# Kernel tuning notes

Measured on AMD Instinct MI355X. Metric: run time of the kernel, lower is better.

Reference implementation:

```python
import jax, jax.numpy as jnp
import numpy as np

B, N, M, D, H = 2, 256, 64, 768, 12
HD = D // H  # head dim 64


def setup_inputs() -> dict:
    key = jax.random.key(0)
    ks = jax.random.split(key, 8)
    s = 0.02
    return {
        "x": jax.random.normal(ks[0], (B, N, D), jnp.float32),
        "sim_embeddings": jax.random.normal(ks[1], (B, N, M, D), jnp.float32),
        "Wq": jax.random.normal(ks[2], (D, D), jnp.float32) * s,
        "bq": jnp.zeros((D,), jnp.float32),
        "Wkv": jax.random.normal(ks[3], (D, 2 * D), jnp.float32) * s,
        "bkv": jnp.zeros((2 * D,), jnp.float32),
        "Wp": jax.random.normal(ks[4], (D, D), jnp.float32) * s,
        "bp": jnp.zeros((D,), jnp.float32),
    }


def reference(x, sim_embeddings, Wq, bq, Wkv, bkv, Wp, bp):
    # x: (B,N,D); sim_embeddings: (B,N,M,D)
    b, n, d = x.shape
    m = sim_embeddings.shape[2]
    scale = HD ** -0.5

    q = (x @ Wq + bq).reshape(b, n, H, HD).transpose(0, 2, 1, 3)  # (B,H,N,hd)

    kv_x = x @ Wkv + bkv                       # (B,N,2D)
    k_x, v_x = jnp.split(kv_x, 2, axis=-1)
    k_x = k_x.reshape(b, n, H, HD).transpose(0, 2, 1, 3)  # (B,H,N,hd) shared-global K
    v_x = v_x.reshape(b, n, H, HD).transpose(0, 2, 1, 3)

    kv_s = sim_embeddings @ Wkv + bkv          # (B,N,M,2D)
    k_s, v_s = jnp.split(kv_s, 2, axis=-1)
    k_s = k_s.reshape(b, n, m, H, HD).transpose(0, 3, 1, 2, 4)  # (B,H,N,M,hd) per-query local K
    v_s = v_s.reshape(b, n, m, H, HD).transpose(0, 3, 1, 2, 4)

    # scores over concatenated [global N keys | local M keys] without expanding K to (B,N,N+M,D)
    sg = jnp.einsum('bhnd,bhkd->bhnk', q, k_x) * scale   # (B,H,N,N)
    sl = jnp.einsum('bhnd,bhnmd->bhnm', q, k_s) * scale  # (B,H,N,M)
    attn = jax.nn.softmax(jnp.concatenate([sg, sl], axis=-1), axis=-1)
    ag, al = attn[..., :n], attn[..., n:]

    out = (jnp.einsum('bhnk,bhkd->bhnd', ag, v_x)
           + jnp.einsum('bhnm,bhnmd->bhnd', al, v_s))   # (B,H,N,hd)
    out = out.transpose(0, 2, 1, 3).reshape(b, n, d)
    return out @ Wp + bp
```

## Files before the change

kernel.cpp:

```cpp
#include <hip/hip_runtime.h>
#include <stdint.h>

#define DEV_INLINE __device__ __forceinline__

typedef __bf16 bf16x8 __attribute__((ext_vector_type(8)));
typedef float f32x4 __attribute__((ext_vector_type(4)));

typedef const __attribute__((address_space(1))) void* gas_ptr;
typedef __attribute__((address_space(3))) void* las_ptr;

DEV_INLINE unsigned short f2bf(float f) {
    union { float f; unsigned u; } v; v.f = f;
    unsigned r = v.u + 0x7fffu + ((v.u >> 16) & 1u);
    return (unsigned short)(r >> 16);
}
DEV_INLINE float bf2f(unsigned short u) {
    union { unsigned u; float f; } v; v.u = ((unsigned)u) << 16;
    return v.f;
}


__global__ void cast_bf16_kernel(const float* __restrict__ src,
                                 unsigned short* __restrict__ dst, long n4) {
    long i = (long)blockIdx.x * blockDim.x + threadIdx.x;
    if (i >= n4) return;
    float4 a = ((const float4*)src)[i];
    ushort4 o;
    o.x = f2bf(a.x); o.y = f2bf(a.y); o.z = f2bf(a.z); o.w = f2bf(a.w);
    ((ushort4*)dst)[i] = o;
}

__global__ void transpose_cast_kernel(const float* __restrict__ src, int C,
                                      unsigned short* __restrict__ dst, int ld_dst) {
    __shared__ float t[64][65];
    int c0 = blockIdx.x * 64, r0 = blockIdx.y * 64;
    int tx = threadIdx.x, ty = threadIdx.y;
    #pragma unroll
    for (int i = 0; i < 64; i += 16)
        t[ty + i][tx] = src[(long)(r0 + ty + i) * C + c0 + tx];
    __syncthreads();
    #pragma unroll
    for (int i = 0; i < 64; i += 16)
        dst[(long)(c0 + ty + i) * ld_dst + r0 + tx] = f2bf(t[tx][ty + i]);
}

__global__ void bias_init_kernel(const float* __restrict__ bq,
                                 const float* __restrict__ bkv,
                                 float* __restrict__ bias1,
                                 float* __restrict__ zerobuf) {
    int i = blockIdx.x * 256 + threadIdx.x;
    if (i < 2304) bias1[i] = (i < 768) ? bq[i] : bkv[i - 768];
    else if (i < 3072) zerobuf[i - 2304] = 0.f;
}


template <int WM, int WN, int WAVES_M, int OUT, bool CIN, bool G1E>
__global__ __launch_bounds__(256)
void gemm_bf16_kernel(const unsigned short* __restrict__ A, int lda,
                      const unsigned short* __restrict__ BT, int ldb,
                      const float* __restrict__ bias,
                      void* __restrict__ Cout, int ldc, int K,
                      const float* __restrict__ cin,
                      long aZb, long aZh, long bZb, long bZh, long oZb, long oZh,
                      float* __restrict__ g1_qf, unsigned short* __restrict__ g1_qb,
                      unsigned short* __restrict__ g1_kxb,
                      unsigned short* __restrict__ g1_vxT) {
    constexpr int TR = WAVES_M * WM * 16;
    constexpr int TC = (4 / WAVES_M) * WN * 16;
    __shared__ unsigned short As[TR * 64];
    __shared__ unsigned short Bs[TC * 64];
    const int tid = threadIdx.x;
    const int w = tid >> 6, lane = tid & 63;
    const int lm = lane & 15, quad = lane >> 4;
    const int z = blockIdx.z;
    const int zb = z / 12, zh = z % 12;
    A  += zb * aZb + zh * aZh;
    BT += zb * bZb + zh * bZh;
    const long obase = zb * oZb + zh * oZh;
    const long tm = (long)blockIdx.y * TR;
    const long tn = (long)blockIdx.x * TC;
    const int m_off = (w % WAVES_M) * WM * 16;
    const int n_off = (w / WAVES_M) * WN * 16;
    const int lrow8 = lane >> 3;
    const int lcol_sw = (((lane & 7) ^ lrow8) * 8);

    f32x4 acc[WM][WN];
    #pragma unroll
    for (int mi = 0; mi < WM; ++mi)
        #pragma unroll
        for (int ni = 0; ni < WN; ++ni) acc[mi][ni] = f32x4{0.f, 0.f, 0.f, 0.f};

    for (int k0 = 0; k0 < K; k0 += 64) {
        __syncthreads();
        #pragma unroll
        for (int i = 0; i < TR / 32; ++i) {
            int r0 = w * (TR / 4) + i * 8;
            const unsigned short* ga = A + (tm + r0 + lrow8) * lda + k0 + lcol_sw;
            __builtin_amdgcn_global_load_lds((gas_ptr)ga, (las_ptr)(As + r0 * 64), 16, 0, 0);
        }
        #pragma unroll
        for (int i = 0; i < TC / 32; ++i) {
            int r0 = w * (TC / 4) + i * 8;
            const unsigned short* gb = BT + (tn + r0 + lrow8) * ldb + k0 + lcol_sw;
            __builtin_amdgcn_global_load_lds((gas_ptr)gb, (las_ptr)(Bs + r0 * 64), 16, 0, 0);
        }
        __syncthreads();
        #pragma unroll
        for (int kk = 0; kk < 2; ++kk) {
            bf16x8 af[WM], bfr[WN];
            #pragma unroll
            for (int mi = 0; mi < WM; ++mi) {
                int r = m_off + mi * 16 + lm;
                af[mi] = *(const bf16x8*)(As + r * 64 + (((kk * 4 + quad) ^ (r & 7)) * 8));
            }
            #pragma unroll
            for (int ni = 0; ni < WN; ++ni) {
                int r = n_off + ni * 16 + lm;
                bfr[ni] = *(const bf16x8*)(Bs + r * 64 + (((kk * 4 + quad) ^ (r & 7)) * 8));
            }
            #pragma unroll
            for (int mi = 0; mi < WM; ++mi)
                #pragma unroll
                for (int ni = 0; ni < WN; ++ni)
                    acc[mi][ni] = __builtin_amdgcn_mfma_f32_16x16x32_bf16(
                        af[mi], bfr[ni], acc[mi][ni], 0, 0, 0);
        }
    }

    #pragma unroll
    for (int mi = 0; mi < WM; ++mi) {
        #pragma unroll
        for (int ni = 0; ni < WN; ++ni) {
            long col = tn + n_off + ni * 16 + lm;
            float bv = bias[col];
            #pragma unroll
            for (int r = 0; r < 4; ++r) {
                long row = tm + m_off + mi * 16 + quad * 4 + r;
                float v = acc[mi][ni][r] + bv;
                if (G1E) {
                    if (col < 768) {
                        g1_qf[row * 768 + col] = v;
                        g1_qb[row * 768 + col] = f2bf(v);
                    } else if (col < 1536) {
                        g1_kxb[row * 768 + (col - 768)] = f2bf(v);
                    } else {
                        int j = (int)col - 1536, h = j >> 6, d = j & 63;
                        int bb = (int)row >> 8, n = (int)row & 255;
                        g1_vxT[((long)(bb * 12 + h) * 64 + d) * 256 + n] = f2bf(v);
                    }
                } else {
                    long idx = obase + row * ldc + col;
                    if (CIN) v += cin[idx];
                    if (OUT == 0) ((float*)Cout)[idx] = v;
                    else ((unsigned short*)Cout)[idx] = f2bf(v);
                }
            }
        }
    }
}

__global__ __launch_bounds__(256)
void attn_fused_kernel(const float* __restrict__ sim,
                       const unsigned short* __restrict__ qWb,
                       const float* __restrict__ qf,
                       const float* __restrict__ bkv,
                       const float* __restrict__ sgbuf,
                       unsigned short* __restrict__ agb,
                       float* __restrict__ outg0,
                       unsigned short* __restrict__ simbar) {
    __shared__ unsigned short qw_s[16 * 784];
    __shared__ unsigned short sim_s[64 * 64];
    __shared__ float q_l[768];
    __shared__ float slb_s[12];
    __shared__ float scl[12][68];
    __shared__ float al_s[12][64];

    const int t = threadIdx.x;
    const int lane = t & 63, w = t >> 6;
    const int lm = lane & 15, quad = lane >> 4;
    const int n = blockIdx.x, b = blockIdx.y;
    const int n_ = b * 256 + n;
    const float* simn = sim + (long)n_ * 49152;

    {
        const int h = t >> 4, c0 = t & 15;
        const unsigned short* src = qWb + ((long)h * 512 + n_) * 768;
        #pragma unroll
        for (int j = 0; j < 6; ++j) {
            int ch = c0 + 16 * j;
            *(bf16x8*)(qw_s + h * 784 + ch * 8) = *(const bf16x8*)(src + ch * 8);
        }
    }
    q_l[t] = qf[(long)n_ * 768 + t];
    q_l[t + 256] = qf[(long)n_ * 768 + t + 256];
    q_l[t + 512] = qf[(long)n_ * 768 + t + 512];
    __syncthreads();
    if (t < 12) {
        float s = 0.f;
        #pragma unroll 8
        for (int d = 0; d < 64; ++d) s += q_l[t * 64 + d] * bkv[t * 64 + d];
        slb_s[t] = s;
    }

    f32x4 acc = {};
    for (int k0 = 0; k0 < 768; k0 += 64) {
        __syncthreads();
        #pragma unroll
        for (int i = 0; i < 2; ++i) {
            int id = t + 256 * i;
            int r = id >> 3, q = id & 7;
            const float* gp = simn + r * 768 + k0 + q * 8;
            float4 a = *(const float4*)gp;
            float4 c = *(const float4*)(gp + 4);
            union { bf16x8 v; unsigned short u[8]; } pk;
            pk.u[0] = f2bf(a.x); pk.u[1] = f2bf(a.y);
            pk.u[2] = f2bf(a.z); pk.u[3] = f2bf(a.w);
            pk.u[4] = f2bf(c.x); pk.u[5] = f2bf(c.y);
            pk.u[6] = f2bf(c.z); pk.u[7] = f2bf(c.w);
            *(bf16x8*)(sim_s + r * 64 + ((q ^ (r & 7)) * 8)) = pk.v;
        }
        __syncthreads();
        #pragma unroll
        for (int kk = 0; kk < 2; ++kk) {
            int r = w * 16 + lm;
            bf16x8 af = *(const bf16x8*)(sim_s + r * 64 + (((kk * 4 + quad) ^ (r & 7)) * 8));
            bf16x8 bf_ = *(const bf16x8*)(qw_s + lm * 784 + k0 + kk * 32 + quad * 8);
            acc = __builtin_amdgcn_mfma_f32_16x16x32_bf16(af, bf_, acc, 0, 0, 0);
        }
    }
    if (lm < 12) {
        #pragma unroll
        for (int r = 0; r < 4; ++r)
            scl[lm][w * 16 + quad * 4 + r] = (acc[r] + slb_s[lm]) * 0.125f;
    }
    __syncthreads();

    #pragma unroll
    for (int i = 0; i < 3; ++i) {
        const int h = w * 3 + i;
        const float* sgr = sgbuf + (long)(b * 12 + h) * 65536 + (long)n * 256;
        float v0 = sgr[lane] * 0.125f, v1 = sgr[lane + 64] * 0.125f,
              v2 = sgr[lane + 128] * 0.125f, v3 = sgr[lane + 192] * 0.125f;
        float v4 = scl[h][lane];
        float mx = fmaxf(fmaxf(fmaxf(v0, v1), fmaxf(v2, v3)), v4);
        #pragma unroll
        for (int off = 32; off > 0; off >>= 1) mx = fmaxf(mx, __shfl_xor(mx, off));
        float e0 = __expf(v0 - mx), e1 = __expf(v1 - mx), e2 = __expf(v2 - mx),
              e3 = __expf(v3 - mx), e4 = __expf(v4 - mx);
        float s = e0 + e1 + e2 + e3 + e4;
        #pragma unroll
        for (int off = 32; off > 0; off >>= 1) s += __shfl_xor(s, off);
        float inv = __frcp_rn(s);
        unsigned short* agr = agb + (long)(b * 12 + h) * 65536 + (long)n * 256;
        agr[lane] = f2bf(e0 * inv); agr[lane + 64] = f2bf(e1 * inv);
        agr[lane + 128] = f2bf(e2 * inv); agr[lane + 192] = f2bf(e3 * inv);
        float al = e4 * inv;
        al_s[h][lane] = al;
        float am = al;
        #pragma unroll
        for (int off = 32; off > 0; off >>= 1) am += __shfl_xor(am, off);
        outg0[(long)n_ * 768 + h * 64 + lane] = am * bkv[768 + h * 64 + lane];
    }
    __syncthreads();

    float a0[12], a1[12], a2[12];
    #pragma unroll
    for (int h = 0; h < 12; ++h) { a0[h] = 0.f; a1[h] = 0.f; a2[h] = 0.f; }
    for (int m = 0; m < 64; ++m) {
        float s0 = simn[(long)m * 768 + t];
        float s1 = simn[(long)m * 768 + t + 256];
        float s2 = simn[(long)m * 768 + t + 512];
        #pragma unroll
        for (int h = 0; h < 12; ++h) {
            float a = al_s[h][m];
            a0[h] += a * s0; a1[h] += a * s1; a2[h] += a * s2;
        }
    }
    #pragma unroll
    for (int h = 0; h < 12; ++h) {
        unsigned short* dst = simbar + ((long)h * 512 + n_) * 768;
        dst[t] = f2bf(a0[h]);
        dst[t + 256] = f2bf(a1[h]);
        dst[t + 512] = f2bf(a2[h]);
    }
}


extern "C" void kernel_launch(void* const* d_in, const int* in_sizes, int n_in,
                              void* d_out, int out_size, void* d_ws, size_t ws_size,
                              hipStream_t stream) {
    const float* x   = (const float*)d_in[0];
    const float* sim = (const float*)d_in[1];
    const float* Wq  = (const float*)d_in[2];
    const float* bq  = (const float*)d_in[3];
    const float* Wkv = (const float*)d_in[4];
    const float* bkv = (const float*)d_in[5];
    const float* Wp  = (const float*)d_in[6];
    const float* bp  = (const float*)d_in[7];
    float* out = (float*)d_out;

    char* ws = (char*)d_ws;
    size_t off = 0;
    auto alloc = [&](size_t bytes) {
        char* p = ws + off;
        off += (bytes + 255) & ~(size_t)255;
        return p;
    };
    unsigned short* xb     = (unsigned short*)alloc(512UL * 768 * 2);
    unsigned short* w1t    = (unsigned short*)alloc(2304UL * 768 * 2);
    unsigned short* wkvb   = (unsigned short*)alloc(768UL * 1536 * 2);
    unsigned short* wpt    = (unsigned short*)alloc(768UL * 768 * 2);
    float*          qf     = (float*)alloc(512UL * 768 * 4);
    unsigned short* qb     = (unsigned short*)alloc(512UL * 768 * 2);
    unsigned short* kxb    = (unsigned short*)alloc(512UL * 768 * 2);
    unsigned short* vxT    = (unsigned short*)alloc(24UL * 64 * 256 * 2);
    unsigned short* qWb    = (unsigned short*)alloc(16UL * 512 * 768 * 2);
    float*          sgbuf  = (float*)alloc(24UL * 65536 * 4);
    unsigned short* agb    = (unsigned short*)alloc(24UL * 65536 * 2);
    float*          outg0  = (float*)alloc(512UL * 768 * 4);
    float*          outg   = (float*)alloc(512UL * 768 * 4);
    unsigned short* simbar = (unsigned short*)alloc(12UL * 512 * 768 * 2);
    unsigned short* attnb  = (unsigned short*)alloc(512UL * 768 * 2);
    float*          bias1  = (float*)alloc(2304UL * 4);
    float*          zbuf   = (float*)alloc(768UL * 4);

    cast_bf16_kernel<<<384, 256, 0, stream>>>(x, xb, 512L * 768 / 4);
    cast_bf16_kernel<<<1152, 256, 0, stream>>>(Wkv, wkvb, 768L * 1536 / 4);
    transpose_cast_kernel<<<dim3(12, 12), dim3(64, 16), 0, stream>>>(Wq, 768, w1t, 768);
    transpose_cast_kernel<<<dim3(24, 12), dim3(64, 16), 0, stream>>>(Wkv, 1536, w1t + 768L * 768, 768);
    transpose_cast_kernel<<<dim3(12, 12), dim3(64, 16), 0, stream>>>(Wp, 768, wpt, 768);
    bias_init_kernel<<<12, 256, 0, stream>>>(bq, bkv, bias1, zbuf);

    gemm_bf16_kernel<2, 2, 2, 0, false, true><<<dim3(36, 8, 1), 256, 0, stream>>>(
        xb, 768, w1t, 768, bias1, nullptr, 768, 768, nullptr,
        0, 0, 0, 0, 0, 0, qf, qb, kxb, vxT);

    gemm_bf16_kernel<2, 2, 2, 1, false, false><<<dim3(12, 8, 12), 256, 0, stream>>>(
        qb, 768, wkvb, 1536, zbuf, qWb, 768, 64, nullptr,
        0, 64, 0, 64, 0, 512L * 768, nullptr, nullptr, nullptr, nullptr);

    gemm_bf16_kernel<2, 2, 2, 0, false, false><<<dim3(4, 4, 24), 256, 0, stream>>>(
        qb, 768, kxb, 768, zbuf, sgbuf, 256, 64, nullptr,
        196608, 64, 196608, 64, 786432, 65536, nullptr, nullptr, nullptr, nullptr);

    attn_fused_kernel<<<dim3(256, 2), 256, 0, stream>>>(
        sim, qWb, qf, bkv, sgbuf, agb, outg0, simbar);

    gemm_bf16_kernel<2, 2, 2, 0, true, false><<<dim3(1, 4, 24), 256, 0, stream>>>(
        agb, 256, vxT, 256, zbuf, outg, 768, 256, outg0,
        786432, 65536, 196608, 16384, 196608, 64, nullptr, nullptr, nullptr, nullptr);

    gemm_bf16_kernel<2, 2, 2, 1, true, false><<<dim3(1, 8, 12), 256, 0, stream>>>(
        simbar, 768, w1t + 1536L * 768, 768, zbuf, attnb, 768, 768, outg,
        0, 393216, 0, 49152, 0, 64, nullptr, nullptr, nullptr, nullptr);

    gemm_bf16_kernel<2, 2, 2, 0, false, false><<<dim3(12, 8, 1), 256, 0, stream>>>(
        attnb, 768, wpt, 768, bp, out, 768, 768, nullptr,
        0, 0, 0, 0, 0, 0, nullptr, nullptr, nullptr, nullptr);
}
```

Before: 252.5 us.

## Merge prep kernels, fuse GEMMs, split simbar, register-prefetch sim tiles

Collapses the cast, transpose and bias kernels into two launches. It merges the qW and sg GEMMs into one grid and fuses the ag·V and simbar·Wv GEMMs into a single concatenated-K GEMM, with smaller tiles for more blocks. The simbar weighted sum moves out of the attention kernel into its own kernel that spreads columns across more blocks. The attention kernel now double-buffers sim tiles through register prefetch with one barrier per chunk. The aim is fewer launches, more parallelism and hidden global-load latency, at the cost of an extra al_g round-trip through global memory and a second full read of sim.

```diff
diff --git a/kernel.cpp b/kernel.cpp
--- a/kernel.cpp
+++ b/kernel.cpp
@@ -14,71 +14,73 @@
     unsigned r = v.u + 0x7fffu + ((v.u >> 16) & 1u);
     return (unsigned short)(r >> 16);
 }
-DEV_INLINE float bf2f(unsigned short u) {
-    union { unsigned u; float f; } v; v.u = ((unsigned)u) << 16;
-    return v.f;
-}
-
-
-__global__ void cast_bf16_kernel(const float* __restrict__ src,
-                                 unsigned short* __restrict__ dst, long n4) {
-    long i = (long)blockIdx.x * blockDim.x + threadIdx.x;
-    if (i >= n4) return;
-    float4 a = ((const float4*)src)[i];
-    ushort4 o;
-    o.x = f2bf(a.x); o.y = f2bf(a.y); o.z = f2bf(a.z); o.w = f2bf(a.w);
-    ((ushort4*)dst)[i] = o;
-}
-
-__global__ void transpose_cast_kernel(const float* __restrict__ src, int C,
-                                      unsigned short* __restrict__ dst, int ld_dst) {
-    __shared__ float t[64][65];
-    int c0 = blockIdx.x * 64, r0 = blockIdx.y * 64;
+
+DEV_INLINE void lds_barrier() {
+    __builtin_amdgcn_sched_barrier(0);
+    asm volatile("s_waitcnt lgkmcnt(0)" ::: "memory");
+    __builtin_amdgcn_s_barrier();
+    __builtin_amdgcn_sched_barrier(0);
+}
+
+__global__ __launch_bounds__(256)
+void prep_cast_kernel(const float* __restrict__ x, unsigned short* __restrict__ xb,
+                      const float* __restrict__ Wkv, unsigned short* __restrict__ wkvb,
+                      const float* __restrict__ bq, const float* __restrict__ bkv,
+                      float* __restrict__ bias1, float* __restrict__ zbuf) {
+    int bid = blockIdx.x;
+    if (bid < 1536) {
+        const float* s; unsigned short* d; long i;
+        if (bid < 384) { s = x;   d = xb;   i = (long)bid * 256 + threadIdx.x; }
+        else           { s = Wkv; d = wkvb; i = (long)(bid - 384) * 256 + threadIdx.x; }
+        float4 a = ((const float4*)s)[i];
+        ushort4 o;
+        o.x = f2bf(a.x); o.y = f2bf(a.y); o.z = f2bf(a.z); o.w = f2bf(a.w);
+        ((ushort4*)d)[i] = o;
+    } else {
+        int i = (bid - 1536) * 256 + threadIdx.x;
+        if (i < 768) bias1[i] = bq[i];
+        else if (i < 2304) bias1[i] = bkv[i - 768];
+        else zbuf[i - 2304] = 0.f;
+    }
+}
+
+__global__ void transpose3_kernel(const float* __restrict__ Wq,
+                                  const float* __restrict__ Wkv,
+                                  const float* __restrict__ Wp,
+                                  unsigned short* __restrict__ w1t,
+                                  unsigned short* __restrict__ wpt) {
+    __shared__ float tl[64][65];
+    int bx = blockIdx.x;
+    const float* src; unsigned short* dst; int C;
+    if (bx < 12)      { src = Wq;  dst = w1t;              C = 768; }
+    else if (bx < 36) { src = Wkv; dst = w1t + 768L * 768; C = 1536; bx -= 12; }
+    else              { src = Wp;  dst = wpt;              C = 768; bx -= 36; }
+    int c0 = bx * 64, r0 = blockIdx.y * 64;
     int tx = threadIdx.x, ty = threadIdx.y;
     #pragma unroll
     for (int i = 0; i < 64; i += 16)
-        t[ty + i][tx] = src[(long)(r0 + ty + i) * C + c0 + tx];
+        tl[ty + i][tx] = src[(long)(r0 + ty + i) * C + c0 + tx];
     __syncthreads();
     #pragma unroll
     for (int i = 0; i < 64; i += 16)
-        dst[(long)(c0 + ty + i) * ld_dst + r0 + tx] = f2bf(t[tx][ty + i]);
-}
-
-__global__ void bias_init_kernel(const float* __restrict__ bq,
-                                 const float* __restrict__ bkv,
-                                 float* __restrict__ bias1,
-                                 float* __restrict__ zerobuf) {
-    int i = blockIdx.x * 256 + threadIdx.x;
-    if (i < 2304) bias1[i] = (i < 768) ? bq[i] : bkv[i - 768];
-    else if (i < 3072) zerobuf[i - 2304] = 0.f;
-}
-
-
-template <int WM, int WN, int WAVES_M, int OUT, bool CIN, bool G1E>
-__global__ __launch_bounds__(256)
-void gemm_bf16_kernel(const unsigned short* __restrict__ A, int lda,
-                      const unsigned short* __restrict__ BT, int ldb,
-                      const float* __restrict__ bias,
-                      void* __restrict__ Cout, int ldc, int K,
-                      const float* __restrict__ cin,
-                      long aZb, long aZh, long bZb, long bZh, long oZb, long oZh,
-                      float* __restrict__ g1_qf, unsigned short* __restrict__ g1_qb,
-                      unsigned short* __restrict__ g1_kxb,
-                      unsigned short* __restrict__ g1_vxT) {
+        dst[(long)(c0 + ty + i) * 768 + r0 + tx] = f2bf(tl[tx][ty + i]);
+}
+
+template <int WM, int WN, int WAVES_M, bool G1E>
+DEV_INLINE void gemm_body(const unsigned short* A, int lda,
+                          const unsigned short* BT, int ldb,
+                          const unsigned short* A2, int lda2,
+                          const unsigned short* B2, int ldb2, int K1,
+                          const float* bias, void* Cout, int ldc, int K,
+                          const float* cin, int OUT, long obase, long tm, long tn,
+                          unsigned short* As, unsigned short* Bs,
+                          float* g1_qf, unsigned short* g1_qb,
+                          unsigned short* g1_kxb, unsigned short* g1_vxT) {
     constexpr int TR = WAVES_M * WM * 16;
     constexpr int TC = (4 / WAVES_M) * WN * 16;
-    __shared__ unsigned short As[TR * 64];
-    __shared__ unsigned short Bs[TC * 64];
     const int tid = threadIdx.x;
     const int w = tid >> 6, lane = tid & 63;
     const int lm = lane & 15, quad = lane >> 4;
-    const int z = blockIdx.z;
-    const int zb = z / 12, zh = z % 12;
-    A  += zb * aZb + zh * aZh;
-    BT += zb * bZb + zh * bZh;
-    const long obase = zb * oZb + zh * oZh;
-    const long tm = (long)blockIdx.y * TR;
-    const long tn = (long)blockIdx.x * TC;
     const int m_off = (w % WAVES_M) * WM * 16;
     const int n_off = (w / WAVES_M) * WN * 16;
     const int lrow8 = lane >> 3;
@@ -91,18 +93,22 @@
         for (int ni = 0; ni < WN; ++ni) acc[mi][ni] = f32x4{0.f, 0.f, 0.f, 0.f};
 
     for (int k0 = 0; k0 < K; k0 += 64) {
+        const unsigned short* Ab; const unsigned short* Bb;
+        int la, lb, kc;
+        if (k0 < K1) { Ab = A;  Bb = BT; la = lda;  lb = ldb;  kc = k0; }
+        else         { Ab = A2; Bb = B2; la = lda2; lb = ldb2; kc = k0 - K1; }
         __syncthreads();
         #pragma unroll
         for (int i = 0; i < TR / 32; ++i) {
-            int r0 = w * (TR / 4) + i * 8;
-            const unsigned short* ga = A + (tm + r0 + lrow8) * lda + k0 + lcol_sw;
-            __builtin_amdgcn_global_load_lds((gas_ptr)ga, (las_ptr)(As + r0 * 64), 16, 0, 0);
+            int rr = w * (TR / 4) + i * 8;
+            const unsigned short* ga = Ab + (tm + rr + lrow8) * la + kc + lcol_sw;
+            __builtin_amdgcn_global_load_lds((gas_ptr)ga, (las_ptr)(As + rr * 64), 16, 0, 0);
         }
         #pragma unroll
         for (int i = 0; i < TC / 32; ++i) {
-            int r0 = w * (TC / 4) + i * 8;
-            const unsigned short* gb = BT + (tn + r0 + lrow8) * ldb + k0 + lcol_sw;
-            __builtin_amdgcn_global_load_lds((gas_ptr)gb, (las_ptr)(Bs + r0 * 64), 16, 0, 0);
+            int rr = w * (TC / 4) + i * 8;
+            const unsigned short* gb = Bb + (tn + rr + lrow8) * lb + kc + lcol_sw;
+            __builtin_amdgcn_global_load_lds((gas_ptr)gb, (las_ptr)(Bs + rr * 64), 16, 0, 0);
         }
         __syncthreads();
         #pragma unroll
@@ -145,18 +151,96 @@
                         g1_kxb[row * 768 + (col - 768)] = f2bf(v);
                     } else {
                         int j = (int)col - 1536, h = j >> 6, d = j & 63;
-                        int bb = (int)row >> 8, n = (int)row & 255;
-                        g1_vxT[((long)(bb * 12 + h) * 64 + d) * 256 + n] = f2bf(v);
+                        int bb = (int)row >> 8, nn = (int)row & 255;
+                        g1_vxT[((long)(bb * 12 + h) * 64 + d) * 256 + nn] = f2bf(v);
                     }
                 } else {
                     long idx = obase + row * ldc + col;
-                    if (CIN) v += cin[idx];
+                    if (cin) v += cin[idx];
                     if (OUT == 0) ((float*)Cout)[idx] = v;
                     else ((unsigned short*)Cout)[idx] = f2bf(v);
                 }
             }
         }
     }
+}
+
+template <int WM, int WN, int WAVES_M, bool G1E>
+__global__ __launch_bounds__(256)
+void gemm_bf16_kernel(const unsigned short* __restrict__ A, int lda,
+                      const unsigned short* __restrict__ BT, int ldb,
+                      const float* __restrict__ bias,
+                      void* __restrict__ Cout, int ldc, int K,
+                      const float* __restrict__ cin, int OUT,
+                      long aZb, long aZh, long bZb, long bZh, long oZb, long oZh,
+                      float* __restrict__ g1_qf, unsigned short* __restrict__ g1_qb,
+                      unsigned short* __restrict__ g1_kxb,
+                      unsigned short* __restrict__ g1_vxT) {
+    constexpr int TR = WAVES_M * WM * 16;
+    constexpr int TC = (4 / WAVES_M) * WN * 16;
+    __shared__ unsigned short As[TR * 64];
+    __shared__ unsigned short Bs[TC * 64];
+    const int z = blockIdx.z, zb = z / 12, zh = z % 12;
+    gemm_body<WM, WN, WAVES_M, G1E>(
+        A + zb * aZb + zh * aZh, lda, BT + zb * bZb + zh * bZh, ldb,
+        nullptr, 0, nullptr, 0, 1 << 30,
+        bias, Cout, ldc, K, cin, OUT, zb * oZb + zh * oZh,
+        (long)blockIdx.y * TR, (long)blockIdx.x * TC, As, Bs,
+        g1_qf, g1_qb, g1_kxb, g1_vxT);
+}
+
+__global__ __launch_bounds__(256)
+void gemm_qwsg_kernel(const unsigned short* __restrict__ qb,
+                      const unsigned short* __restrict__ wkvb,
+                      const unsigned short* __restrict__ kxb,
+                      const float* __restrict__ zbuf,
+                      unsigned short* __restrict__ qWb,
+                      float* __restrict__ sgbuf) {
+    __shared__ unsigned short As[64 * 64];
+    __shared__ unsigned short Bs[64 * 64];
+    int bid = blockIdx.x;
+    if (bid < 1152) {
+        int bx = bid % 12, by = (bid / 12) % 8, h = bid / 96;
+        gemm_body<2, 2, 2, false>(
+            qb + h * 64, 768, wkvb + h * 64, 1536,
+            nullptr, 0, nullptr, 0, 1 << 30,
+            zbuf, qWb, 768, 64, nullptr, 1, (long)h * 393216,
+            (long)by * 64, (long)bx * 64, As, Bs,
+            nullptr, nullptr, nullptr, nullptr);
+    } else {
+        int bid2 = bid - 1152;
+        int bx = bid2 % 4, by = (bid2 / 4) % 4, z = bid2 / 16;
+        int zb = z / 12, zh = z % 12;
+        gemm_body<2, 2, 2, false>(
+            qb + zb * 196608 + zh * 64, 768, kxb + zb * 196608 + zh * 64, 768,
+            nullptr, 0, nullptr, 0, 1 << 30,
+            zbuf, sgbuf, 256, 64, nullptr, 0,
+            (long)zb * 786432 + (long)zh * 65536,
+            (long)by * 64, (long)bx * 64, As, Bs,
+            nullptr, nullptr, nullptr, nullptr);
+    }
+}
+
+template <int WM, int WN, int WAVES_M>
+__global__ __launch_bounds__(256)
+void gemm_concat_kernel(const unsigned short* __restrict__ A, int lda, long aZb, long aZh,
+                        const unsigned short* __restrict__ BT, int ldb, long bZb, long bZh,
+                        const unsigned short* __restrict__ A2, int lda2, long a2Zb, long a2Zh,
+                        const unsigned short* __restrict__ B2, int ldb2, long b2Zb, long b2Zh,
+                        int K1, int K, const float* __restrict__ bias,
+                        void* __restrict__ Cout, int ldc,
+                        const float* __restrict__ cin, int OUT, long oZb, long oZh) {
+    constexpr int TR = WAVES_M * WM * 16;
+    constexpr int TC = (4 / WAVES_M) * WN * 16;
+    __shared__ unsigned short As[TR * 64];
+    __shared__ unsigned short Bs[TC * 64];
+    const int z = blockIdx.z, zb = z / 12, zh = z % 12;
+    gemm_body<WM, WN, WAVES_M, false>(
+        A + zb * aZb + zh * aZh, lda, BT + zb * bZb + zh * bZh, ldb,
+        A2 + zb * a2Zb + zh * a2Zh, lda2, B2 + zb * b2Zb + zh * b2Zh, ldb2, K1,
+        bias, Cout, ldc, K, cin, OUT, zb * oZb + zh * oZh,
+        (long)blockIdx.y * TR, (long)blockIdx.x * TC, As, Bs,
+        nullptr, nullptr, nullptr, nullptr);
 }
 
 __global__ __launch_bounds__(256)
@@ -167,13 +251,12 @@
                        const float* __restrict__ sgbuf,
                        unsigned short* __restrict__ agb,
                        float* __restrict__ outg0,
-                       unsigned short* __restrict__ simbar) {
+                       float* __restrict__ al_g) {
     __shared__ unsigned short qw_s[16 * 784];
-    __shared__ unsigned short sim_s[64 * 64];
+    __shared__ unsigned short sim_s[2][64 * 64];
     __shared__ float q_l[768];
     __shared__ float slb_s[12];
     __shared__ float scl[12][68];
-    __shared__ float al_s[12][64];
 
     const int t = threadIdx.x;
     const int lane = t & 63, w = t >> 6;
@@ -194,6 +277,15 @@
     q_l[t] = qf[(long)n_ * 768 + t];
     q_l[t + 256] = qf[(long)n_ * 768 + t + 256];
     q_l[t + 512] = qf[(long)n_ * 768 + t + 512];
+
+    const int r0 = t >> 3, q8 = t & 7, r1 = r0 + 32;
+    float4 p0a, p0b, p1a, p1b;
+    {
+        const float* g0 = simn + r0 * 768 + q8 * 8;
+        p0a = *(const float4*)g0; p0b = *(const float4*)(g0 + 4);
+        const float* g1 = simn + r1 * 768 + q8 * 8;
+        p1a = *(const float4*)g1; p1b = *(const float4*)(g1 + 4);
+    }
     __syncthreads();
     if (t < 12) {
         float s = 0.f;
@@ -203,29 +295,34 @@
     }
 
     f32x4 acc = {};
-    for (int k0 = 0; k0 < 768; k0 += 64) {
-        __syncthreads();
-        #pragma unroll
-        for (int i = 0; i < 2; ++i) {
-            int id = t + 256 * i;
-            int r = id >> 3, q = id & 7;
-            const float* gp = simn + r * 768 + k0 + q * 8;
-            float4 a = *(const float4*)gp;
-            float4 c = *(const float4*)(gp + 4);
-            union { bf16x8 v; unsigned short u[8]; } pk;
-            pk.u[0] = f2bf(a.x); pk.u[1] = f2bf(a.y);
-            pk.u[2] = f2bf(a.z); pk.u[3] = f2bf(a.w);
-            pk.u[4] = f2bf(c.x); pk.u[5] = f2bf(c.y);
-            pk.u[6] = f2bf(c.z); pk.u[7] = f2bf(c.w);
-            *(bf16x8*)(sim_s + r * 64 + ((q ^ (r & 7)) * 8)) = pk.v;
-        }
-        __syncthreads();
+    #pragma unroll
+    for (int c = 0; c < 12; ++c) {
+        const int k0 = c * 64;
+        unsigned short* buf = sim_s[c & 1];
+        union { bf16x8 v; unsigned short u[8]; } pk;
+        pk.u[0] = f2bf(p0a.x); pk.u[1] = f2bf(p0a.y);
+        pk.u[2] = f2bf(p0a.z); pk.u[3] = f2bf(p0a.w);
+        pk.u[4] = f2bf(p0b.x); pk.u[5] = f2bf(p0b.y);
+        pk.u[6] = f2bf(p0b.z); pk.u[7] = f2bf(p0b.w);
+        *(bf16x8*)(buf + r0 * 64 + ((q8 ^ (r0 & 7)) * 8)) = pk.v;
+        pk.u[0] = f2bf(p1a.x); pk.u[1] = f2bf(p1a.y);
+        pk.u[2] = f2bf(p1a.z); pk.u[3] = f2bf(p1a.w);
+        pk.u[4] = f2bf(p1b.x); pk.u[5] = f2bf(p1b.y);
+        pk.u[6] = f2bf(p1b.z); pk.u[7] = f2bf(p1b.w);
+        *(bf16x8*)(buf + r1 * 64 + ((q8 ^ (r1 & 7)) * 8)) = pk.v;
+        if (c < 11) {
+            const float* g0 = simn + r0 * 768 + k0 + 64 + q8 * 8;
+            p0a = *(const float4*)g0; p0b = *(const float4*)(g0 + 4);
+            const float* g1 = simn + r1 * 768 + k0 + 64 + q8 * 8;
+            p1a = *(const float4*)g1; p1b = *(const float4*)(g1 + 4);
+        }
+        lds_barrier();
         #pragma unroll
         for (int kk = 0; kk < 2; ++kk) {
             int r = w * 16 + lm;
-            bf16x8 af = *(const bf16x8*)(sim_s + r * 64 + (((kk * 4 + quad) ^ (r & 7)) * 8));
-            bf16x8 bf_ = *(const bf16x8*)(qw_s + lm * 784 + k0 + kk * 32 + quad * 8);
-            acc = __builtin_amdgcn_mfma_f32_16x16x32_bf16(af, bf_, acc, 0, 0, 0);
+            bf16x8 af = *(const bf16x8*)(buf + r * 64 + (((kk * 4 + quad) ^ (r & 7)) * 8));
+            bf16x8 bfr = *(const bf16x8*)(qw_s + lm * 784 + k0 + kk * 32 + quad * 8);
+            acc = __builtin_amdgcn_mfma_f32_16x16x32_bf16(af, bfr, acc, 0, 0, 0);
         }
     }
     if (lm < 12) {
@@ -255,34 +352,39 @@
         agr[lane] = f2bf(e0 * inv); agr[lane + 64] = f2bf(e1 * inv);
         agr[lane + 128] = f2bf(e2 * inv); agr[lane + 192] = f2bf(e3 * inv);
         float al = e4 * inv;
-        al_s[h][lane] = al;
+        al_g[(long)n_ * 768 + h * 64 + lane] = al;
         float am = al;
         #pragma unroll
         for (int off = 32; off > 0; off >>= 1) am += __shfl_xor(am, off);
         outg0[(long)n_ * 768 + h * 64 + lane] = am * bkv[768 + h * 64 + lane];
     }
+}
+
+__global__ __launch_bounds__(256)
+void simbar_kernel(const float* __restrict__ sim,
+                   const float* __restrict__ al_g,
+                   unsigned short* __restrict__ simbar) {
+    __shared__ float al_l[768];
+    const int t = threadIdx.x;
+    const int n_ = blockIdx.x;
+    const int c = blockIdx.y * 256 + t;
+    const float* simn = sim + (long)n_ * 49152;
+    al_l[t] = al_g[(long)n_ * 768 + t];
+    al_l[t + 256] = al_g[(long)n_ * 768 + t + 256];
+    al_l[t + 512] = al_g[(long)n_ * 768 + t + 512];
     __syncthreads();
-
-    float a0[12], a1[12], a2[12];
-    #pragma unroll
-    for (int h = 0; h < 12; ++h) { a0[h] = 0.f; a1[h] = 0.f; a2[h] = 0.f; }
+    float a[12];
+    #pragma unroll
+    for (int h = 0; h < 12; ++h) a[h] = 0.f;
+    #pragma unroll 4
     for (int m = 0; m < 64; ++m) {
-        float s0 = simn[(long)m * 768 + t];
-        float s1 = simn[(long)m * 768 + t + 256];
-        float s2 = simn[(long)m * 768 + t + 512];
-        #pragma unroll
-        for (int h = 0; h < 12; ++h) {
-            float a = al_s[h][m];
-            a0[h] += a * s0; a1[h] += a * s1; a2[h] += a * s2;
-        }
-    }
-    #pragma unroll
-    for (int h = 0; h < 12; ++h) {
-        unsigned short* dst = simbar + ((long)h * 512 + n_) * 768;
-        dst[t] = f2bf(a0[h]);
-        dst[t + 256] = f2bf(a1[h]);
-        dst[t + 512] = f2bf(a2[h]);
-    }
+        float s = simn[(long)m * 768 + c];
+        #pragma unroll
+        for (int h = 0; h < 12; ++h) a[h] += al_l[h * 64 + m] * s;
+    }
+    #pragma unroll
+    for (int h = 0; h < 12; ++h)
+        simbar[((long)h * 512 + n_) * 768 + c] = f2bf(a[h]);
 }
 
 
@@ -318,43 +420,34 @@
     float*          sgbuf  = (float*)alloc(24UL * 65536 * 4);
     unsigned short* agb    = (unsigned short*)alloc(24UL * 65536 * 2);
     float*          outg0  = (float*)alloc(512UL * 768 * 4);
-    float*          outg   = (float*)alloc(512UL * 768 * 4);
+    float*          al_g   = (float*)alloc(512UL * 768 * 4);
     unsigned short* simbar = (unsigned short*)alloc(12UL * 512 * 768 * 2);
     unsigned short* attnb  = (unsigned short*)alloc(512UL * 768 * 2);
     float*          bias1  = (float*)alloc(2304UL * 4);
     float*          zbuf   = (float*)alloc(768UL * 4);
 
-    cast_bf16_kernel<<<384, 256, 0, stream>>>(x, xb, 512L * 768 / 4);
-    cast_bf16_kernel<<<1152, 256, 0, stream>>>(Wkv, wkvb, 768L * 1536 / 4);
-    transpose_cast_kernel<<<dim3(12, 12), dim3(64, 16), 0, stream>>>(Wq, 768, w1t, 768);
-    transpose_cast_kernel<<<dim3(24, 12), dim3(64, 16), 0, stream>>>(Wkv, 1536, w1t + 768L * 768, 768);
-    transpose_cast_kernel<<<dim3(12, 12), dim3(64, 16), 0, stream>>>(Wp, 768, wpt, 768);
-    bias_init_kernel<<<12, 256, 0, stream>>>(bq, bkv, bias1, zbuf);
-
-    gemm_bf16_kernel<2, 2, 2, 0, false, true><<<dim3(36, 8, 1), 256, 0, stream>>>(
-        xb, 768, w1t, 768, bias1, nullptr, 768, 768, nullptr,
+    prep_cast_kernel<<<1548, 256, 0, stream>>>(x, xb, Wkv, wkvb, bq, bkv, bias1, zbuf);
+    transpose3_kernel<<<dim3(48, 12), dim3(64, 16), 0, stream>>>(Wq, Wkv, Wp, w1t, wpt);
+
+    gemm_bf16_kernel<2, 2, 2, true><<<dim3(36, 8, 1), 256, 0, stream>>>(
+        xb, 768, w1t, 768, bias1, nullptr, 768, 768, nullptr, 0,
         0, 0, 0, 0, 0, 0, qf, qb, kxb, vxT);
 
-    gemm_bf16_kernel<2, 2, 2, 1, false, false><<<dim3(12, 8, 12), 256, 0, stream>>>(
-        qb, 768, wkvb, 1536, zbuf, qWb, 768, 64, nullptr,
-        0, 64, 0, 64, 0, 512L * 768, nullptr, nullptr, nullptr, nullptr);
-
-    gemm_bf16_kernel<2, 2, 2, 0, false, false><<<dim3(4, 4, 24), 256, 0, stream>>>(
-        qb, 768, kxb, 768, zbuf, sgbuf, 256, 64, nullptr,
-        196608, 64, 196608, 64, 786432, 65536, nullptr, nullptr, nullptr, nullptr);
+    gemm_qwsg_kernel<<<1536, 256, 0, stream>>>(qb, wkvb, kxb, zbuf, qWb, sgbuf);
 
     attn_fused_kernel<<<dim3(256, 2), 256, 0, stream>>>(
-        sim, qWb, qf, bkv, sgbuf, agb, outg0, simbar);
-
-    gemm_bf16_kernel<2, 2, 2, 0, true, false><<<dim3(1, 4, 24), 256, 0, stream>>>(
-        agb, 256, vxT, 256, zbuf, outg, 768, 256, outg0,
-        786432, 65536, 196608, 16384, 196608, 64, nullptr, nullptr, nullptr, nullptr);
-
-    gemm_bf16_kernel<2, 2, 2, 1, true, false><<<dim3(1, 8, 12), 256, 0, stream>>>(
-        simbar, 768, w1t + 1536L * 768, 768, zbuf, attnb, 768, 768, outg,
-        0, 393216, 0, 49152, 0, 64, nullptr, nullptr, nullptr, nullptr);
-
-    gemm_bf16_kernel<2, 2, 2, 0, false, false><<<dim3(12, 8, 1), 256, 0, stream>>>(
-        attnb, 768, wpt, 768, bp, out, 768, 768, nullptr,
+        sim, qWb, qf, bkv, sgbuf, agb, outg0, al_g);
+
+    simbar_kernel<<<dim3(512, 3), 256, 0, stream>>>(sim, al_g, simbar);
+
+    gemm_concat_kernel<1, 1, 2><<<dim3(2, 8, 24), 256, 0, stream>>>(
+        simbar, 768, 196608, 393216,
+        w1t + 1536L * 768, 768, 0, 49152,
+        agb, 256, 786432, 65536,
+        vxT, 256, 196608, 16384,
+        768, 1024, zbuf, attnb, 768, outg0, 1, 196608, 64);
+
+    gemm_bf16_kernel<1, 1, 2, false><<<dim3(24, 16, 1), 256, 0, stream>>>(
+        attnb, 768, wpt, 768, bp, out, 768, 768, nullptr, 0,
         0, 0, 0, 0, 0, 0, nullptr, nullptr, nullptr, nullptr);
 }
```

Result: faster. 241.0 us (-4.6%).
